# Kernel optimization log

Measured on AMD Instinct MI355X. Metric: run time of the kernel, lower is better.

The kernel has to match this reference:

```python
import jax, jax.numpy as jnp
import numpy as np

B, S, E = 8, 2048, 512

def setup_inputs() -> dict:
    key = jax.random.key(0)
    ks = jax.random.split(key, 7)
    Q = jax.random.normal(ks[0], (B, S, E), dtype=jnp.float32)
    K = jax.random.normal(ks[1], (B, S, E), dtype=jnp.float32)
    pad_mask = jax.random.randint(ks[2], (B, S, S), 0, 2).astype(bool)
    # torch nn.Linear weights are [out, in]; y = x @ W.T + b
    sc = 1.0 / np.sqrt(E)
    Wq = jax.random.uniform(ks[3], (E, E), jnp.float32, -sc, sc)
    Wk = jax.random.uniform(ks[4], (E, E), jnp.float32, -sc, sc)
    Wv = jax.random.uniform(ks[5], (E, E), jnp.float32, -sc, sc)
    Wp = jax.random.uniform(ks[6], (E, E), jnp.float32, -sc, sc)
    bp = jnp.zeros((E,), jnp.float32)
    return {"Q": Q, "K": K, "pad_mask": pad_mask, "Wq": Wq, "Wk": Wk, "Wv": Wv, "Wp": Wp, "bp": bp}

def reference(Q, K, pad_mask, Wq, Wk, Wv, Wp, bp):
    scale = E ** (-0.5)
    V = K  # V aliases K before projection, as in the original
    q = jnp.einsum('bse,fe->bsf', Q, Wq)   # q_map (no bias)
    k = jnp.einsum('bse,fe->bsf', K, Wk)   # k_map
    v = jnp.einsum('bse,fe->bsf', V, Wv)   # v_map
    scores = jnp.einsum('bqe,bke->bqk', q, k) * scale  # [B,S,S]
    scores = jnp.where(pad_mask, -1e9, scores)
    attn = jax.nn.softmax(scores, axis=-1)
    out = jnp.einsum('bqk,bke->bqe', attn, v)
    out = jnp.einsum('bse,fe->bsf', out, Wp) + bp       # proj
    return q + out  # residual uses projected Q (faithful to source)
```

## Files before the change

### kernel.cpp

```cpp
#include <hip/hip_runtime.h>
#include <hip/hip_bf16.h>

typedef short v8s __attribute__((ext_vector_type(8)));
typedef float v4f __attribute__((ext_vector_type(4)));

static constexpr int BB = 8, SS = 2048, EE = 512;

enum { EPI_BF16 = 0, EPI_SCALE = 1, EPI_FINAL = 2 };

struct EpiParams {
  float scale;
  const float* bias;
  const __hip_bfloat16* resid;
  int resid_ld;
};

static constexpr int SMEM_BYTES = 34816;

struct CastParams {
  const float* src[4];
  __hip_bfloat16* dst[4];
};

__global__ __launch_bounds__(256) void cast_weights(CastParams cp) {
  const int seg = blockIdx.x >> 7;
  const int b = blockIdx.x & 127;
  const float* x = cp.src[seg] + (unsigned long long)b * 2048;
  __hip_bfloat16* y = cp.dst[seg] + (unsigned long long)b * 2048;
  int i = threadIdx.x * 8;
  float4 f0 = ((const float4*)(x + i))[0];
  float4 f1 = ((const float4*)(x + i))[1];
  alignas(16) __hip_bfloat16 h[8];
  h[0] = __float2bfloat16(f0.x); h[1] = __float2bfloat16(f0.y);
  h[2] = __float2bfloat16(f0.z); h[3] = __float2bfloat16(f0.w);
  h[4] = __float2bfloat16(f1.x); h[5] = __float2bfloat16(f1.y);
  h[6] = __float2bfloat16(f1.z); h[7] = __float2bfloat16(f1.w);
  *(uint4*)(y + i) = *(uint4*)h;
}

__device__ __forceinline__ void stage_tile64(const __hip_bfloat16* __restrict__ G,
                                             int row0, int ld, int k0,
                                             __hip_bfloat16* lds, int wave, int lane) {
#pragma unroll
  for (int t = 0; t < 4; ++t) {
    const int p = (wave * 4 + t) * 64 + lane;
    const int row = p >> 3;
    const int g = (p & 7) ^ (row & 7);
    const __hip_bfloat16* src = G + (unsigned long long)(row0 + row) * ld + k0 + g * 8;
    __builtin_amdgcn_global_load_lds(
        (const __attribute__((address_space(1))) void*)src,
        (__attribute__((address_space(3))) void*)(lds + (wave * 4 + t) * 512),
        16, 0, 0);
  }
}

__device__ __forceinline__ void stage_tile64_f32(const float* __restrict__ G,
                                                 int row0, int ld, int k0,
                                                 __hip_bfloat16* lds, int tid) {
#pragma unroll
  for (int c = 0; c < 4; ++c) {
    const int p = c * 256 + tid;
    const int row = p >> 3;
    const int g = (p & 7) ^ (row & 7);
    const float* src = G + (unsigned long long)(row0 + row) * ld + k0 + g * 8;
    float4 f0 = ((const float4*)src)[0];
    float4 f1 = ((const float4*)src)[1];
    alignas(16) __hip_bfloat16 h[8];
    h[0] = __float2bfloat16(f0.x); h[1] = __float2bfloat16(f0.y);
    h[2] = __float2bfloat16(f0.z); h[3] = __float2bfloat16(f0.w);
    h[4] = __float2bfloat16(f1.x); h[5] = __float2bfloat16(f1.y);
    h[6] = __float2bfloat16(f1.z); h[7] = __float2bfloat16(f1.w);
    *(uint4*)&lds[p * 8] = *(uint4*)h;
  }
}

template <int EPI, bool AF32, bool BF32>
__device__ __forceinline__ void gemm_body(const void* Agv, const void* Bgv,
                                          void* Cg, int K, int lda, int ldb, int ldc,
                                          int m0, int n0, const EpiParams& ep,
                                          unsigned char* smem) {
  __hip_bfloat16* As = (__hip_bfloat16*)smem;
  __hip_bfloat16* Bs = As + 128 * 64;

  const int tid = threadIdx.x;
  const int lane = tid & 63;
  const int wave = tid >> 6;
  const int wr = wave >> 1;
  const int wc = wave & 1;

  v4f acc[4][4];
  const v4f vzero = {0.f, 0.f, 0.f, 0.f};
#pragma unroll
  for (int i = 0; i < 4; ++i)
#pragma unroll
    for (int j = 0; j < 4; ++j) acc[i][j] = vzero;

  const int fr = lane & 15;
  const int fq = lane >> 4;

  for (int k0 = 0; k0 < K; k0 += 64) {
    __syncthreads();
    if constexpr (AF32)
      stage_tile64_f32((const float*)Agv, m0, lda, k0, As, tid);
    else
      stage_tile64((const __hip_bfloat16*)Agv, m0, lda, k0, As, wave, lane);
    if constexpr (BF32)
      stage_tile64_f32((const float*)Bgv, n0, ldb, k0, Bs, tid);
    else
      stage_tile64((const __hip_bfloat16*)Bgv, n0, ldb, k0, Bs, wave, lane);
    __syncthreads();

#pragma unroll
    for (int ks = 0; ks < 2; ++ks) {
      const int gq = ks * 4 + fq;
      v8s a[4], b[4];
#pragma unroll
      for (int i = 0; i < 4; ++i) {
        const int r = wr * 64 + i * 16 + fr;
        a[i] = *(const v8s*)&As[r * 64 + ((gq ^ (r & 7)) * 8)];
      }
#pragma unroll
      for (int j = 0; j < 4; ++j) {
        const int r = wc * 64 + j * 16 + fr;
        b[j] = *(const v8s*)&Bs[r * 64 + ((gq ^ (r & 7)) * 8)];
      }
#pragma unroll
      for (int i = 0; i < 4; ++i)
#pragma unroll
        for (int j = 0; j < 4; ++j)
          acc[i][j] = __builtin_amdgcn_mfma_f32_16x16x32_bf16(a[i], b[j], acc[i][j], 0, 0, 0);
    }
  }

  const int cf = lane & 15;
  const int rq = (lane >> 4) * 4;

  __syncthreads();

  if constexpr (EPI != EPI_FINAL) {
    __hip_bfloat16* Ct = (__hip_bfloat16*)smem;
    const int ST = 136;
#pragma unroll
    for (int i = 0; i < 4; ++i) {
      const int rl = wr * 64 + i * 16 + rq;
#pragma unroll
      for (int j = 0; j < 4; ++j) {
        const int col = wc * 64 + j * 16 + cf;
#pragma unroll
        for (int r = 0; r < 4; ++r) {
          float v = acc[i][j][r];
          if constexpr (EPI == EPI_SCALE) v *= ep.scale;
          Ct[(rl + r) * ST + col] = __float2bfloat16(v);
        }
      }
    }
    __syncthreads();
    __hip_bfloat16* C = (__hip_bfloat16*)Cg;
#pragma unroll
    for (int c = 0; c < 8; ++c) {
      const int idx = c * 256 + tid;
      const int row = idx >> 4;
      const int colc = (idx & 15) * 8;
      *(v8s*)&C[(unsigned long long)(m0 + row) * ldc + n0 + colc] =
          *(const v8s*)&Ct[row * ST + colc];
    }
  } else {
    float* Cf = (float*)smem;
    const int ST = 132;
    float* C = (float*)Cg;
#pragma unroll
    for (int h = 0; h < 2; ++h) {
      if (wr == h) {
#pragma unroll
        for (int i = 0; i < 4; ++i) {
          const int rl = i * 16 + rq;
#pragma unroll
          for (int j = 0; j < 4; ++j) {
            const int col = wc * 64 + j * 16 + cf;
#pragma unroll
            for (int r = 0; r < 4; ++r) Cf[(rl + r) * ST + col] = acc[i][j][r];
          }
        }
      }
      __syncthreads();
#pragma unroll
      for (int c = 0; c < 8; ++c) {
        const int idx = c * 256 + tid;
        const int row = idx >> 5;
        const int colc = (idx & 31) * 4;
        const int grow = m0 + h * 64 + row;
        const int gcol = n0 + colc;
        float4 v = *(const float4*)&Cf[row * ST + colc];
        float4 b4 = *(const float4*)&ep.bias[gcol];
        ushort4 r4 = *(const ushort4*)&ep.resid[(unsigned long long)grow * ep.resid_ld + gcol];
        v.x += b4.x + __bfloat162float(*(__hip_bfloat16*)&r4.x);
        v.y += b4.y + __bfloat162float(*(__hip_bfloat16*)&r4.y);
        v.z += b4.z + __bfloat162float(*(__hip_bfloat16*)&r4.z);
        v.w += b4.w + __bfloat162float(*(__hip_bfloat16*)&r4.w);
        *(float4*)&C[(unsigned long long)grow * ldc + gcol] = v;
      }
      if (h == 0) __syncthreads();
    }
  }
}

template <int EPI>
__global__ __launch_bounds__(256, 3) void gemm_bt(
    const __hip_bfloat16* __restrict__ Ag, const __hip_bfloat16* __restrict__ Bg,
    void* __restrict__ Cg, int K, int lda, int ldb, int ldc,
    unsigned long long sAz, unsigned long long sBz, unsigned long long sCz, EpiParams ep) {
  __shared__ __align__(16) unsigned char smem[SMEM_BYTES];
  const unsigned long long z = blockIdx.z;
  void* Cz;
  if constexpr (EPI == EPI_FINAL) Cz = (void*)((float*)Cg + z * sCz);
  else Cz = (void*)((__hip_bfloat16*)Cg + z * sCz);
  gemm_body<EPI, false, false>(Ag + z * sAz, Bg + z * sBz, Cz, K, lda, ldb, ldc,
                               blockIdx.y * 128, blockIdx.x * 128, ep, smem);
}

__global__ __launch_bounds__(256, 3) void gemm_qkv(
    const float* __restrict__ Q, const float* __restrict__ K,
    const __hip_bfloat16* __restrict__ Wq, const __hip_bfloat16* __restrict__ Wk,
    const __hip_bfloat16* __restrict__ Wv,
    __hip_bfloat16* __restrict__ qb, __hip_bfloat16* __restrict__ kb,
    __hip_bfloat16* __restrict__ vT) {
  __shared__ __align__(16) unsigned char smem[SMEM_BYTES];
  const int z = blockIdx.z;
  EpiParams ep{};
  if (z == 2) {
    gemm_body<EPI_BF16, false, true>(Wv, K, vT, EE, EE, EE, BB * SS,
                                     blockIdx.y * 128, blockIdx.x * 128, ep, smem);
  } else {
    const float* A = (z == 0) ? Q : K;
    const __hip_bfloat16* B = (z == 0) ? Wq : Wk;
    __hip_bfloat16* C = (z == 0) ? qb : kb;
    gemm_body<EPI_BF16, true, false>(A, B, C, EE, EE, EE, EE,
                                     blockIdx.x * 128, blockIdx.y * 128, ep, smem);
  }
}

static constexpr int FLASH_LDS = 147968;

__device__ __forceinline__ void stage_K64(const __hip_bfloat16* __restrict__ Kb, int kv0,
                                          __hip_bfloat16* lds, int tid) {
  const int wv = tid >> 6;
#pragma unroll
  for (int c = 0; c < 8; ++c) {
    const int p = c * 512 + tid;
    const int chunk = p >> 9;
    const int row = (p >> 3) & 63;
    const int g = (p & 7) ^ (row & 7);
    const __hip_bfloat16* src = Kb + (unsigned long long)(kv0 + row) * 512ull + chunk * 64 + g * 8;
    __builtin_amdgcn_global_load_lds(
        (const __attribute__((address_space(1))) void*)src,
        (__attribute__((address_space(3))) void*)(lds + (c * 512 + wv * 64) * 8),
        16, 0, 0);
  }
}

__global__ __launch_bounds__(512, 2) void flash_attn(
    const __hip_bfloat16* __restrict__ qb, const __hip_bfloat16* __restrict__ kb,
    const __hip_bfloat16* __restrict__ vT, const unsigned char* __restrict__ mask,
    __hip_bfloat16* __restrict__ ob) {
  extern __shared__ __align__(16) char fsm[];
  __hip_bfloat16* Ks0 = (__hip_bfloat16*)fsm;
  __hip_bfloat16* Ps0 = (__hip_bfloat16*)(fsm + 131072);
  float* lred = (float*)(fsm + 147456);

  const int tid = threadIdx.x;
  const int lane = tid & 63;
  const int w = tid >> 6;
  const int fr = lane & 15;
  const int fq = lane >> 4;
  const int wq = w & 3;
  const int wk = w >> 2;
  const int b = blockIdx.x & 7;
  const int q0 = (blockIdx.x >> 3) * 64;
  const unsigned long long bS = (unsigned long long)b * 2048ull;
  const float SC = 0.044194173824159216f;

  v8s qf[16];
  {
    const __hip_bfloat16* qrow = qb + (bS + q0 + wq * 16 + fr) * 512ull;
#pragma unroll
    for (int kk = 0; kk < 16; ++kk) qf[kk] = *(const v8s*)&qrow[kk * 32 + fq * 8];
  }

  v4f acc[4][4];
  const v4f vz = {0.f, 0.f, 0.f, 0.f};
#pragma unroll
  for (int i = 0; i < 4; ++i)
#pragma unroll
    for (int j = 0; j < 4; ++j) acc[i][j] = vz;

  float lsum[4] = {0.f, 0.f, 0.f, 0.f};

  const __hip_bfloat16* Kb = kb + bS * 512ull;
  const unsigned char* Mb = mask + (bS + q0) * 2048ull;

  stage_K64(Kb, 0, Ks0, tid);

  unsigned char mkc[2][4];
#pragma unroll
  for (int j = 0; j < 2; ++j)
#pragma unroll
    for (int r = 0; r < 4; ++r)
      mkc[j][r] = Mb[(unsigned long long)(wq * 16 + fq * 4 + r) * 2048ull + wk * 32 + j * 16 + fr];

  __syncthreads();

  for (int t = 0; t < 32; ++t) {
    __hip_bfloat16* KsT = Ks0 + (t & 1) * 32768;
    __hip_bfloat16* PsT = Ps0 + (t & 1) * 4096;
    const int kv0 = t * 64;

    if (t < 31) stage_K64(Kb, (t + 1) * 64, Ks0 + ((t + 1) & 1) * 32768, tid);

    unsigned char mkn[2][4] = {};
    if (t < 31) {
#pragma unroll
      for (int j = 0; j < 2; ++j)
#pragma unroll
        for (int r = 0; r < 4; ++r)
          mkn[j][r] = Mb[(unsigned long long)(wq * 16 + fq * 4 + r) * 2048ull +
                         kv0 + 64 + wk * 32 + j * 16 + fr];
    }

    v8s vb[2][4];
#pragma unroll
    for (int ks = 0; ks < 2; ++ks)
#pragma unroll
      for (int j = 0; j < 4; ++j)
        vb[ks][j] = *(const v8s*)&vT[(unsigned long long)(w * 64 + j * 16 + fr) * 16384ull +
                                     bS + kv0 + ks * 32 + fq * 8];

    v4f sa[2][2] = {{vz, vz}, {vz, vz}};
    __builtin_amdgcn_s_setprio(1);
#pragma unroll
    for (int kk2 = 0; kk2 < 8; ++kk2)
#pragma unroll
      for (int par = 0; par < 2; ++par) {
        const int kk = kk2 * 2 + par;
#pragma unroll
        for (int j = 0; j < 2; ++j) {
          const int rr = wk * 32 + j * 16 + fr;
          v8s kf = *(const v8s*)&KsT[(kk >> 1) * 4096 + rr * 64 + ((((kk & 1) * 4 + fq) ^ (rr & 7)) * 8)];
          sa[j][par] = __builtin_amdgcn_mfma_f32_16x16x32_bf16(qf[kk], kf, sa[j][par], 0, 0, 0);
        }
      }
    __builtin_amdgcn_s_setprio(0);

#pragma unroll
    for (int j = 0; j < 2; ++j) {
      const int col = wk * 32 + j * 16 + fr;
      const int cg = col >> 3, cl = col & 7;
#pragma unroll
      for (int r = 0; r < 4; ++r) {
        const float s = mkc[j][r] ? -1e9f : (sa[j][0][r] + sa[j][1][r]) * SC;
        const float p = __expf(s);
        lsum[r] += p;
        const int row = wq * 16 + fq * 4 + r;
        PsT[row * 64 + ((cg ^ (row & 7)) * 8) + cl] = __float2bfloat16(p);
      }
    }
#pragma unroll
    for (int j = 0; j < 2; ++j)
#pragma unroll
      for (int r = 0; r < 4; ++r) mkc[j][r] = mkn[j][r];

    asm volatile("s_waitcnt vmcnt(0) lgkmcnt(0)" ::: "memory");
    __builtin_amdgcn_s_barrier();
    __builtin_amdgcn_sched_barrier(0);

    __builtin_amdgcn_s_setprio(1);
#pragma unroll
    for (int ks = 0; ks < 2; ++ks) {
      v8s pa[4];
#pragma unroll
      for (int i = 0; i < 4; ++i) {
        const int row = i * 16 + fr;
        pa[i] = *(const v8s*)&PsT[row * 64 + (((ks * 4 + fq) ^ (row & 7)) * 8)];
      }
#pragma unroll
      for (int i = 0; i < 4; ++i)
#pragma unroll
        for (int j = 0; j < 4; ++j)
          acc[i][j] = __builtin_amdgcn_mfma_f32_16x16x32_bf16(pa[i], vb[ks][j], acc[i][j], 0, 0, 0);
    }
    __builtin_amdgcn_s_setprio(0);
  }

#pragma unroll
  for (int off = 1; off <= 8; off <<= 1)
#pragma unroll
    for (int r = 0; r < 4; ++r) lsum[r] += __shfl_xor(lsum[r], off);
  if (fr == 0)
    *(float4*)&lred[wk * 64 + wq * 16 + fq * 4] = make_float4(lsum[0], lsum[1], lsum[2], lsum[3]);
  __syncthreads();

#pragma unroll
  for (int i = 0; i < 4; ++i) {
#pragma unroll
    for (int r = 0; r < 4; ++r) {
      const int row = i * 16 + fq * 4 + r;
      const float den = lred[row] + lred[64 + row];
      const float inv = den > 0.f ? 1.f / den : 0.f;
      __hip_bfloat16* orow = ob + (bS + q0 + row) * 512ull + w * 64 + fr;
#pragma unroll
      for (int j = 0; j < 4; ++j)
        orow[j * 16] = __float2bfloat16(acc[i][j][r] * inv);
    }
  }
}

extern "C" void kernel_launch(void* const* d_in, const int* in_sizes, int n_in,
                              void* d_out, int out_size, void* d_ws, size_t ws_size,
                              hipStream_t stream) {
  const float* Q = (const float*)d_in[0];
  const float* K = (const float*)d_in[1];
  const unsigned char* mask = (const unsigned char*)d_in[2];
  const float* Wq = (const float*)d_in[3];
  const float* Wk = (const float*)d_in[4];
  const float* Wv = (const float*)d_in[5];
  const float* Wp = (const float*)d_in[6];
  const float* bp = (const float*)d_in[7];
  float* out = (float*)d_out;

  char* ws = (char*)d_ws;
  const unsigned long long MB = 1024ull * 1024ull;
  __hip_bfloat16* qb = (__hip_bfloat16*)(ws + 0 * MB);
  __hip_bfloat16* kb = (__hip_bfloat16*)(ws + 16 * MB);
  __hip_bfloat16* vT = (__hip_bfloat16*)(ws + 32 * MB);
  __hip_bfloat16* Wqb = (__hip_bfloat16*)(ws + 48 * MB);
  __hip_bfloat16* Wkb = Wqb + 512 * 512;
  __hip_bfloat16* Wvb = Wkb + 512 * 512;
  __hip_bfloat16* Wpb = Wvb + 512 * 512;
  __hip_bfloat16* ob = (__hip_bfloat16*)(ws + 64 * MB);

  dim3 blk(256, 1, 1);

  CastParams cp;
  cp.src[0] = Wq; cp.dst[0] = Wqb;
  cp.src[1] = Wk; cp.dst[1] = Wkb;
  cp.src[2] = Wv; cp.dst[2] = Wvb;
  cp.src[3] = Wp; cp.dst[3] = Wpb;
  cast_weights<<<dim3(512, 1, 1), blk, 0, stream>>>(cp);

  gemm_qkv<<<dim3((BB * SS) / 128, EE / 128, 3), blk, 0, stream>>>(
      Q, K, Wqb, Wkb, Wvb, qb, kb, vT);

  static bool attr_done = false;
  if (!attr_done) {
    hipFuncSetAttribute((const void*)flash_attn,
                        hipFuncAttributeMaxDynamicSharedMemorySize, FLASH_LDS);
    attr_done = true;
  }
  flash_attn<<<dim3(256, 1, 1), dim3(512, 1, 1), FLASH_LDS, stream>>>(
      qb, kb, vT, mask, ob);

  EpiParams epf{};
  epf.bias = bp;
  epf.resid = qb;
  epf.resid_ld = EE;
  gemm_bt<EPI_FINAL><<<dim3(EE / 128, (BB * SS) / 128, 1), blk, 0, stream>>>(
      ob, Wpb, out, EE, EE, EE, EE, 0ull, 0ull, 0ull, epf);
}
```

Baseline: 387.0 us.

## Fold V projection into output projection via precomputed Wp·Wv

```diff
diff --git a/kernel.cpp b/kernel.cpp
--- a/kernel.cpp
+++ b/kernel.cpp
@@ -38,6 +38,33 @@
   *(uint4*)(y + i) = *(uint4*)h;
 }
 
+__global__ __launch_bounds__(256) void transpose_cast(
+    const float* __restrict__ src, __hip_bfloat16* __restrict__ dst,
+    int src_ld, int dst_ld, unsigned long long src_zstride, int dst_zoff_stride) {
+  __shared__ float tile[64][68];
+  const int C0 = blockIdx.x * 64;
+  const int R0 = blockIdx.y * 64;
+  const unsigned long long zs = (unsigned long long)blockIdx.z * src_zstride;
+  const int zo = blockIdx.z * dst_zoff_stride;
+  const int t = threadIdx.x;
+  const int r = t >> 2;
+  const int c4 = (t & 3) * 16;
+
+  const float* s = src + zs + (unsigned long long)(R0 + r) * src_ld + C0 + c4;
+  *(float4*)&tile[r][c4 + 0]  = ((const float4*)s)[0];
+  *(float4*)&tile[r][c4 + 4]  = ((const float4*)s)[1];
+  *(float4*)&tile[r][c4 + 8]  = ((const float4*)s)[2];
+  *(float4*)&tile[r][c4 + 12] = ((const float4*)s)[3];
+  __syncthreads();
+
+  alignas(16) __hip_bfloat16 h[16];
+#pragma unroll
+  for (int k = 0; k < 16; ++k) h[k] = __float2bfloat16(tile[c4 + k][r]);
+  __hip_bfloat16* d = dst + (unsigned long long)(C0 + r) * dst_ld + zo + R0 + c4;
+  ((uint4*)d)[0] = ((uint4*)h)[0];
+  ((uint4*)d)[1] = ((uint4*)h)[1];
+}
+
 __device__ __forceinline__ void stage_tile64(const __hip_bfloat16* __restrict__ G,
                                              int row0, int ld, int k0,
                                              __hip_bfloat16* lds, int wave, int lane) {
@@ -218,25 +245,18 @@
                                blockIdx.y * 128, blockIdx.x * 128, ep, smem);
 }
 
-__global__ __launch_bounds__(256, 3) void gemm_qkv(
+__global__ __launch_bounds__(256, 3) void gemm_qk(
     const float* __restrict__ Q, const float* __restrict__ K,
     const __hip_bfloat16* __restrict__ Wq, const __hip_bfloat16* __restrict__ Wk,
-    const __hip_bfloat16* __restrict__ Wv,
-    __hip_bfloat16* __restrict__ qb, __hip_bfloat16* __restrict__ kb,
-    __hip_bfloat16* __restrict__ vT) {
+    __hip_bfloat16* __restrict__ qb, __hip_bfloat16* __restrict__ kb) {
   __shared__ __align__(16) unsigned char smem[SMEM_BYTES];
   const int z = blockIdx.z;
   EpiParams ep{};
-  if (z == 2) {
-    gemm_body<EPI_BF16, false, true>(Wv, K, vT, EE, EE, EE, BB * SS,
-                                     blockIdx.y * 128, blockIdx.x * 128, ep, smem);
-  } else {
-    const float* A = (z == 0) ? Q : K;
-    const __hip_bfloat16* B = (z == 0) ? Wq : Wk;
-    __hip_bfloat16* C = (z == 0) ? qb : kb;
-    gemm_body<EPI_BF16, true, false>(A, B, C, EE, EE, EE, EE,
-                                     blockIdx.x * 128, blockIdx.y * 128, ep, smem);
-  }
+  const float* A = (z == 0) ? Q : K;
+  const __hip_bfloat16* B = (z == 0) ? Wq : Wk;
+  __hip_bfloat16* C = (z == 0) ? qb : kb;
+  gemm_body<EPI_BF16, true, false>(A, B, C, EE, EE, EE, EE,
+                                   blockIdx.x * 128, blockIdx.y * 128, ep, smem);
 }
 
 static constexpr int FLASH_LDS = 147968;
@@ -428,26 +448,36 @@
 
   char* ws = (char*)d_ws;
   const unsigned long long MB = 1024ull * 1024ull;
-  __hip_bfloat16* qb = (__hip_bfloat16*)(ws + 0 * MB);
-  __hip_bfloat16* kb = (__hip_bfloat16*)(ws + 16 * MB);
-  __hip_bfloat16* vT = (__hip_bfloat16*)(ws + 32 * MB);
+  __hip_bfloat16* qb  = (__hip_bfloat16*)(ws + 0 * MB);
+  __hip_bfloat16* kb  = (__hip_bfloat16*)(ws + 16 * MB);
+  __hip_bfloat16* kbT = (__hip_bfloat16*)(ws + 32 * MB);
   __hip_bfloat16* Wqb = (__hip_bfloat16*)(ws + 48 * MB);
   __hip_bfloat16* Wkb = Wqb + 512 * 512;
-  __hip_bfloat16* Wvb = Wkb + 512 * 512;
-  __hip_bfloat16* Wpb = Wvb + 512 * 512;
-  __hip_bfloat16* ob = (__hip_bfloat16*)(ws + 64 * MB);
+  __hip_bfloat16* Wpb = Wkb + 512 * 512;
+  __hip_bfloat16* WvT = Wpb + 512 * 512;
+  __hip_bfloat16* Ntb = WvT + 512 * 512;
+  __hip_bfloat16* ob  = (__hip_bfloat16*)(ws + 64 * MB);
 
   dim3 blk(256, 1, 1);
 
   CastParams cp;
   cp.src[0] = Wq; cp.dst[0] = Wqb;
   cp.src[1] = Wk; cp.dst[1] = Wkb;
-  cp.src[2] = Wv; cp.dst[2] = Wvb;
+  cp.src[2] = Wp; cp.dst[2] = Wpb;
   cp.src[3] = Wp; cp.dst[3] = Wpb;
-  cast_weights<<<dim3(512, 1, 1), blk, 0, stream>>>(cp);
-
-  gemm_qkv<<<dim3((BB * SS) / 128, EE / 128, 3), blk, 0, stream>>>(
-      Q, K, Wqb, Wkb, Wvb, qb, kb, vT);
+  cast_weights<<<dim3(384, 1, 1), blk, 0, stream>>>(cp);
+
+  transpose_cast<<<dim3(8, 8, 1), blk, 0, stream>>>(Wv, WvT, 512, 512, 0ull, 0);
+
+  transpose_cast<<<dim3(8, 32, 8), blk, 0, stream>>>(
+      K, kbT, 512, BB * SS, (unsigned long long)SS * EE, SS);
+
+  EpiParams epn{};
+  gemm_bt<EPI_BF16><<<dim3(4, 4, 1), blk, 0, stream>>>(
+      Wpb, WvT, Ntb, EE, EE, EE, EE, 0ull, 0ull, 0ull, epn);
+
+  gemm_qk<<<dim3((BB * SS) / 128, EE / 128, 2), blk, 0, stream>>>(
+      Q, K, Wqb, Wkb, qb, kb);
 
   static bool attr_done = false;
   if (!attr_done) {
@@ -456,12 +486,12 @@
     attr_done = true;
   }
   flash_attn<<<dim3(256, 1, 1), dim3(512, 1, 1), FLASH_LDS, stream>>>(
-      qb, kb, vT, mask, ob);
+      qb, kb, kbT, mask, ob);
 
   EpiParams epf{};
   epf.bias = bp;
   epf.resid = qb;
   epf.resid_ld = EE;
   gemm_bt<EPI_FINAL><<<dim3(EE / 128, (BB * SS) / 128, 1), blk, 0, stream>>>(
-      ob, Wpb, out, EE, EE, EE, EE, 0ull, 0ull, 0ull, epf);
-}
+      ob, Ntb, out, EE, EE, EE, EE, 0ull, 0ull, 0ull, epf);
+}
```

After: 398.9 us. 1.03x slower.
